# Kernel optimization log

Hardware: AMD Instinct MI355X
Metric: run time of the kernel (lower is better)

Reference implementation:

```python
import jax, jax.numpy as jnp
import numpy as np

B, S, D, H = 4, 2048, 512, 8
HD = D // H
SCALE = jnp.sqrt(jnp.float32(HD))


def setup_inputs() -> dict:
    key = jax.random.key(0)
    ks = jax.random.split(key, 13)
    s = 0.02
    return {
        "Q": jax.random.normal(ks[0], (B, S, D), jnp.float32),
        "K": jax.random.normal(ks[1], (B, S, D), jnp.float32),
        "V": jax.random.normal(ks[2], (B, S, D), jnp.float32),
        "mask": jax.random.randint(ks[3], (B, 1, S, S), 0, 2).astype(bool),
        "Wq": jax.random.normal(ks[4], (D, D), jnp.float32) * s,
        "bq": jnp.zeros((D,), jnp.float32),
        "Wk": jax.random.normal(ks[5], (D, D), jnp.float32) * s,
        "bk": jnp.zeros((D,), jnp.float32),
        "Wv": jax.random.normal(ks[6], (D, D), jnp.float32) * s,
        "bv": jnp.zeros((D,), jnp.float32),
        "Wo": jax.random.normal(ks[7], (D, D), jnp.float32) * s,
        "bo": jnp.zeros((D,), jnp.float32),
    }


def reference(Q, K, V, mask, Wq, bq, Wk, bk, Wv, bv, Wo, bo):
    b, s, d = Q.shape
    # torch Linear: x @ W^T + b
    q = (Q @ Wq.T + bq).reshape(b, s, H, HD).transpose(0, 2, 1, 3)  # [B,H,S,HD]
    k = (K @ Wk.T + bk).reshape(b, s, H, HD).transpose(0, 2, 1, 3)
    v = (V @ Wv.T + bv).reshape(b, s, H, HD).transpose(0, 2, 1, 3)
    scores = jnp.einsum('bhqd,bhkd->bhqk', q, k) / SCALE  # [B,H,S,S]
    scores = jnp.where(mask, jnp.float32(-1e10), scores)
    dist = jax.nn.softmax(scores, axis=-1)
    attn = jnp.einsum('bhqk,bhkd->bhqd', dist, v)
    x = attn.transpose(0, 2, 1, 3).reshape(b, s, d)
    x = x @ Wo.T + bo
    return x, dist
```

## Files before the change

kernel.cpp:

```cpp
#include <hip/hip_runtime.h>
#include <hip/hip_bf16.h>
#include <math.h>

#define B 4
#define S 2048
#define D 512
#define H 8
#define HD 64
#define M_TOT (B * S)
#define X_SIZE (B * S * D)
#define STRIDE_BH (S * HD)
#define STRIDE_B (H * S * HD)
#define SW64 (S / 64)

typedef __attribute__((ext_vector_type(8))) short bf16x8;
typedef __attribute__((ext_vector_type(4))) float f32x4;

__global__ __launch_bounds__(256) void cvt_all(
    const float* __restrict__ Q, const float* __restrict__ K,
    const float* __restrict__ V, const float* __restrict__ Wq,
    const float* __restrict__ Wk, const float* __restrict__ Wv,
    const float* __restrict__ Wo, __hip_bfloat16* __restrict__ outb) {
  const int NX = X_SIZE / 8;
  const int NW = (D * D) / 8;
  const int total = 3 * NX + 4 * NW;
  int c = blockIdx.x * 256 + threadIdx.x;
  const int stride = gridDim.x * 256;
  for (; c < total; c += stride) {
    const float* src;
    int off;
    if (c < NX)          { src = Q;  off = c; }
    else if (c < 2 * NX) { src = K;  off = c - NX; }
    else if (c < 3 * NX) { src = V;  off = c - 2 * NX; }
    else {
      int wc = c - 3 * NX;
      int wi = wc >> 15;
      src = (wi == 0) ? Wq : (wi == 1) ? Wk : (wi == 2) ? Wv : Wo;
      off = wc & (NW - 1);
    }
    const float4 x0 = *(const float4*)&src[(size_t)off * 8];
    const float4 x1 = *(const float4*)&src[(size_t)off * 8 + 4];
    bf16x8 pk;
    __hip_bfloat16* p = (__hip_bfloat16*)&pk;
    p[0] = __float2bfloat16(x0.x); p[1] = __float2bfloat16(x0.y);
    p[2] = __float2bfloat16(x0.z); p[3] = __float2bfloat16(x0.w);
    p[4] = __float2bfloat16(x1.x); p[5] = __float2bfloat16(x1.y);
    p[6] = __float2bfloat16(x1.z); p[7] = __float2bfloat16(x1.w);
    *(bf16x8*)&outb[(size_t)c * 8] = pk;
  }
}

__global__ __launch_bounds__(256) void mask_pack(
    const int* __restrict__ mask, unsigned long long* __restrict__ mbits) {
  const int lane = threadIdx.x & 63;
  const int wid = threadIdx.x >> 6;
  const size_t nwords = (size_t)B * S * SW64;
  size_t w = (size_t)blockIdx.x * 4 + wid;
  const size_t stride = (size_t)gridDim.x * 4;
  for (; w < nwords; w += stride) {
    int m = mask[w * 64 + lane];
    unsigned long long bits = __ballot(m != 0);
    if (lane == 0) mbits[w] = bits;
  }
}

template <int TRANS>
__global__ __launch_bounds__(256) void gemm_proj(
    const __hip_bfloat16* __restrict__ X, const __hip_bfloat16* __restrict__ W,
    const float* __restrict__ bias, __hip_bfloat16* __restrict__ out) {
  __shared__ __hip_bfloat16 As[64][72];
  __shared__ __hip_bfloat16 Bs[64][72];
  const int tid = threadIdx.x;
  const int lane = tid & 63;
  const int wave = tid >> 6;
  const int wr = wave >> 1, wc = wave & 1;
  const int l15 = lane & 15, quad = lane >> 4;
  const int h = blockIdx.x;
  const int n0 = h * 64;
  const int m0 = blockIdx.y * 64;

  f32x4 acc[2][2] = {};

  for (int k0 = 0; k0 < D; k0 += 64) {
#pragma unroll
    for (int i = 0; i < 2; ++i) {
      int idx = tid + i * 256;
      int r = idx >> 3, c8 = idx & 7;
      *(bf16x8*)&As[r][c8 * 8] = *(const bf16x8*)&X[(size_t)(m0 + r) * D + k0 + c8 * 8];
      *(bf16x8*)&Bs[r][c8 * 8] = *(const bf16x8*)&W[(size_t)(n0 + r) * D + k0 + c8 * 8];
    }
    __syncthreads();

    bf16x8 a[2][2], b[2][2];
#pragma unroll
    for (int mf = 0; mf < 2; ++mf) {
      a[mf][0] = *(const bf16x8*)&As[wr * 32 + mf * 16 + l15][quad * 8];
      a[mf][1] = *(const bf16x8*)&As[wr * 32 + mf * 16 + l15][32 + quad * 8];
    }
#pragma unroll
    for (int nf = 0; nf < 2; ++nf) {
      b[nf][0] = *(const bf16x8*)&Bs[wc * 32 + nf * 16 + l15][quad * 8];
      b[nf][1] = *(const bf16x8*)&Bs[wc * 32 + nf * 16 + l15][32 + quad * 8];
    }
#pragma unroll
    for (int mf = 0; mf < 2; ++mf)
#pragma unroll
      for (int nf = 0; nf < 2; ++nf) {
        if (TRANS) {
          acc[mf][nf] = __builtin_amdgcn_mfma_f32_16x16x32_bf16(b[nf][0], a[mf][0], acc[mf][nf], 0, 0, 0);
          acc[mf][nf] = __builtin_amdgcn_mfma_f32_16x16x32_bf16(b[nf][1], a[mf][1], acc[mf][nf], 0, 0, 0);
        } else {
          acc[mf][nf] = __builtin_amdgcn_mfma_f32_16x16x32_bf16(a[mf][0], b[nf][0], acc[mf][nf], 0, 0, 0);
          acc[mf][nf] = __builtin_amdgcn_mfma_f32_16x16x32_bf16(a[mf][1], b[nf][1], acc[mf][nf], 0, 0, 0);
        }
      }
    __syncthreads();
  }

  if (!TRANS) {
#pragma unroll
    for (int mf = 0; mf < 2; ++mf)
#pragma unroll
      for (int r = 0; r < 4; ++r) {
        int m = m0 + wr * 32 + mf * 16 + quad * 4 + r;
        int bb = m >> 11, s = m & 2047;
        __hip_bfloat16* obh = out + (size_t)bb * STRIDE_B + (size_t)h * STRIDE_BH;
#pragma unroll
        for (int nf = 0; nf < 2; ++nf) {
          int hd = wc * 32 + nf * 16 + l15;
          obh[(size_t)s * HD + hd] =
              __float2bfloat16(acc[mf][nf][r] + bias[n0 + hd]);
        }
      }
  } else {
#pragma unroll
    for (int mf = 0; mf < 2; ++mf)
#pragma unroll
      for (int r = 0; r < 4; ++r)
#pragma unroll
        for (int nf = 0; nf < 2; ++nf) {
          int hd = wc * 32 + nf * 16 + quad * 4 + r;
          int m = m0 + wr * 32 + mf * 16 + l15;
          int bb = m >> 11, s = m & 2047;
          __hip_bfloat16* obh = out + (size_t)bb * STRIDE_B + (size_t)h * STRIDE_BH;
          obh[(size_t)hd * S + s] =
              __float2bfloat16(acc[mf][nf][r] + bias[n0 + hd]);
        }
  }
}

__global__ __launch_bounds__(256) void attn_fused(
    const __hip_bfloat16* __restrict__ q, const __hip_bfloat16* __restrict__ k,
    const __hip_bfloat16* __restrict__ vT,
    const unsigned long long* __restrict__ mbits,
    float* __restrict__ dist, __hip_bfloat16* __restrict__ attn) {
  __shared__ __hip_bfloat16 ps[4][16][72];

  const int tid = threadIdx.x;
  const int wave = tid >> 6;
  const int lane = tid & 63;
  const int l15 = lane & 15;
  const int quad = lane >> 4;
  const int qt = blockIdx.x >> 5;
  const int bh = blockIdx.x & 31;
  const int b = bh >> 3;
  const int row0 = qt * 64 + wave * 16;

  const __hip_bfloat16* qb  = q  + (size_t)bh * STRIDE_BH;
  const __hip_bfloat16* kb  = k  + (size_t)bh * STRIDE_BH;
  const __hip_bfloat16* vtb = vT + (size_t)bh * STRIDE_BH;
  const unsigned long long* mb64 = mbits + (size_t)b * S * SW64;
  float* distb = dist + (size_t)bh * S * S;
  __hip_bfloat16* af = attn + (size_t)b * S * D + (size_t)(bh & 7) * HD;

  const bf16x8 qf0 = *(const bf16x8*)(qb + (size_t)(row0 + l15) * HD + quad * 8);
  const bf16x8 qf1 = *(const bf16x8*)(qb + (size_t)(row0 + l15) * HD + 32 + quad * 8);

  float lpart[4] = {0.f, 0.f, 0.f, 0.f};

  for (int kt = 0; kt < 32; ++kt) {
    const int col0 = kt * 64;
    unsigned long long mw[4];
#pragma unroll
    for (int r = 0; r < 4; ++r)
      mw[r] = mb64[(size_t)(row0 + quad * 4 + r) * SW64 + kt];
#pragma unroll
    for (int ct = 0; ct < 4; ++ct) {
      const int col = col0 + ct * 16 + l15;
      const bf16x8 kf0 = *(const bf16x8*)(kb + (size_t)col * HD + quad * 8);
      const bf16x8 kf1 = *(const bf16x8*)(kb + (size_t)col * HD + 32 + quad * 8);
      f32x4 s = {0.f, 0.f, 0.f, 0.f};
      s = __builtin_amdgcn_mfma_f32_16x16x32_bf16(qf0, kf0, s, 0, 0, 0);
      s = __builtin_amdgcn_mfma_f32_16x16x32_bf16(qf1, kf1, s, 0, 0, 0);
#pragma unroll
      for (int r = 0; r < 4; ++r) {
        int msk = (int)((mw[r] >> (ct * 16 + l15)) & 1ull);
        float e = msk ? 0.f : __expf(s[r] * 0.125f);
        lpart[r] += e;
      }
    }
  }
#pragma unroll
  for (int r = 0; r < 4; ++r) {
    float v = lpart[r];
    v += __shfl_xor(v, 1, 64);
    v += __shfl_xor(v, 2, 64);
    v += __shfl_xor(v, 4, 64);
    v += __shfl_xor(v, 8, 64);
    lpart[r] = 1.0f / v;
  }

  f32x4 oacc[4] = {{0.f, 0.f, 0.f, 0.f}, {0.f, 0.f, 0.f, 0.f},
                   {0.f, 0.f, 0.f, 0.f}, {0.f, 0.f, 0.f, 0.f}};
  for (int kt = 0; kt < 32; ++kt) {
    const int col0 = kt * 64;
    unsigned long long mw[4];
#pragma unroll
    for (int r = 0; r < 4; ++r)
      mw[r] = mb64[(size_t)(row0 + quad * 4 + r) * SW64 + kt];
#pragma unroll
    for (int ct = 0; ct < 4; ++ct) {
      const int col = col0 + ct * 16 + l15;
      const bf16x8 kf0 = *(const bf16x8*)(kb + (size_t)col * HD + quad * 8);
      const bf16x8 kf1 = *(const bf16x8*)(kb + (size_t)col * HD + 32 + quad * 8);
      f32x4 s = {0.f, 0.f, 0.f, 0.f};
      s = __builtin_amdgcn_mfma_f32_16x16x32_bf16(qf0, kf0, s, 0, 0, 0);
      s = __builtin_amdgcn_mfma_f32_16x16x32_bf16(qf1, kf1, s, 0, 0, 0);
#pragma unroll
      for (int r = 0; r < 4; ++r) {
        int row = row0 + quad * 4 + r;
        int msk = (int)((mw[r] >> (ct * 16 + l15)) & 1ull);
        float e = msk ? 0.f : __expf(s[r] * 0.125f);
        float p = e * lpart[r];
        __builtin_nontemporal_store(p, &distb[(size_t)row * S + col]);
        ps[wave][quad * 4 + r][ct * 16 + l15] = __float2bfloat16(p);
      }
    }
    const bf16x8 pa0 = *(const bf16x8*)&ps[wave][l15][quad * 8];
    const bf16x8 pa1 = *(const bf16x8*)&ps[wave][l15][32 + quad * 8];
#pragma unroll
    for (int ct = 0; ct < 4; ++ct) {
      const __hip_bfloat16* vrow = vtb + (size_t)(ct * 16 + l15) * S + col0;
      const bf16x8 vf0 = *(const bf16x8*)(vrow + quad * 8);
      const bf16x8 vf1 = *(const bf16x8*)(vrow + 32 + quad * 8);
      oacc[ct] = __builtin_amdgcn_mfma_f32_16x16x32_bf16(pa0, vf0, oacc[ct], 0, 0, 0);
      oacc[ct] = __builtin_amdgcn_mfma_f32_16x16x32_bf16(pa1, vf1, oacc[ct], 0, 0, 0);
    }
  }

#pragma unroll
  for (int ct = 0; ct < 4; ++ct)
#pragma unroll
    for (int r = 0; r < 4; ++r) {
      int row = row0 + quad * 4 + r;
      af[(size_t)row * D + ct * 16 + l15] = __float2bfloat16(oacc[ct][r]);
    }
}

__global__ __launch_bounds__(256) void gemm_out(
    const __hip_bfloat16* __restrict__ Abf, const __hip_bfloat16* __restrict__ W,
    const float* __restrict__ bias, float* __restrict__ outp) {
  __shared__ __hip_bfloat16 As[64][72];
  __shared__ __hip_bfloat16 Bs[64][72];
  const int tid = threadIdx.x;
  const int lane = tid & 63;
  const int wave = tid >> 6;
  const int wr = wave >> 1, wc = wave & 1;
  const int l15 = lane & 15, quad = lane >> 4;
  const int n0 = blockIdx.x * 64;
  const int m0 = blockIdx.y * 64;

  f32x4 acc[2][2] = {};

  for (int k0 = 0; k0 < D; k0 += 64) {
#pragma unroll
    for (int i = 0; i < 2; ++i) {
      int idx = tid + i * 256;
      int r = idx >> 3, c8 = idx & 7;
      *(bf16x8*)&As[r][c8 * 8] = *(const bf16x8*)&Abf[(size_t)(m0 + r) * D + k0 + c8 * 8];
      *(bf16x8*)&Bs[r][c8 * 8] = *(const bf16x8*)&W[(size_t)(n0 + r) * D + k0 + c8 * 8];
    }
    __syncthreads();

    bf16x8 a[2][2], b[2][2];
#pragma unroll
    for (int mf = 0; mf < 2; ++mf) {
      a[mf][0] = *(const bf16x8*)&As[wr * 32 + mf * 16 + l15][quad * 8];
      a[mf][1] = *(const bf16x8*)&As[wr * 32 + mf * 16 + l15][32 + quad * 8];
    }
#pragma unroll
    for (int nf = 0; nf < 2; ++nf) {
      b[nf][0] = *(const bf16x8*)&Bs[wc * 32 + nf * 16 + l15][quad * 8];
      b[nf][1] = *(const bf16x8*)&Bs[wc * 32 + nf * 16 + l15][32 + quad * 8];
    }
#pragma unroll
    for (int mf = 0; mf < 2; ++mf)
#pragma unroll
      for (int nf = 0; nf < 2; ++nf) {
        acc[mf][nf] = __builtin_amdgcn_mfma_f32_16x16x32_bf16(a[mf][0], b[nf][0], acc[mf][nf], 0, 0, 0);
        acc[mf][nf] = __builtin_amdgcn_mfma_f32_16x16x32_bf16(a[mf][1], b[nf][1], acc[mf][nf], 0, 0, 0);
      }
    __syncthreads();
  }

#pragma unroll
  for (int mf = 0; mf < 2; ++mf)
#pragma unroll
    for (int r = 0; r < 4; ++r) {
      int m = m0 + wr * 32 + mf * 16 + quad * 4 + r;
#pragma unroll
      for (int nf = 0; nf < 2; ++nf) {
        int n = n0 + wc * 32 + nf * 16 + l15;
        outp[(size_t)m * D + n] = acc[mf][nf][r] + bias[n];
      }
    }
}

extern "C" void kernel_launch(void* const* d_in, const int* in_sizes, int n_in,
                              void* d_out, int out_size, void* d_ws, size_t ws_size,
                              hipStream_t stream) {
  const float* Q    = (const float*)d_in[0];
  const float* K    = (const float*)d_in[1];
  const float* V    = (const float*)d_in[2];
  const int*   mask = (const int*)d_in[3];
  const float* Wq   = (const float*)d_in[4];
  const float* bq   = (const float*)d_in[5];
  const float* Wk   = (const float*)d_in[6];
  const float* bk   = (const float*)d_in[7];
  const float* Wv   = (const float*)d_in[8];
  const float* bv   = (const float*)d_in[9];
  const float* Wo   = (const float*)d_in[10];
  const float* bo   = (const float*)d_in[11];

  float* x_out = (float*)d_out;
  float* dist  = x_out + (size_t)X_SIZE;

  __hip_bfloat16* cvtb = (__hip_bfloat16*)d_ws;
  __hip_bfloat16* Qb   = cvtb;
  __hip_bfloat16* Kb   = Qb + (size_t)X_SIZE;
  __hip_bfloat16* Vb   = Kb + (size_t)X_SIZE;
  __hip_bfloat16* Wqb  = Vb + (size_t)X_SIZE;
  __hip_bfloat16* Wkb  = Wqb + (size_t)D * D;
  __hip_bfloat16* Wvb  = Wkb + (size_t)D * D;
  __hip_bfloat16* Wob  = Wvb + (size_t)D * D;
  __hip_bfloat16* qb   = Wob + (size_t)D * D;
  __hip_bfloat16* kbf  = qb + (size_t)X_SIZE;
  __hip_bfloat16* vtb  = kbf + (size_t)X_SIZE;
  unsigned long long* mbits = (unsigned long long*)(vtb + (size_t)X_SIZE);
  __hip_bfloat16* abf  = Qb;

  dim3 blk(256);
  dim3 g(D / 64, M_TOT / 64);

  cvt_all<<<dim3(2048), blk, 0, stream>>>(Q, K, V, Wq, Wk, Wv, Wo, cvtb);
  mask_pack<<<dim3(1024), blk, 0, stream>>>(mask, mbits);
  gemm_proj<0><<<g, blk, 0, stream>>>(Qb, Wqb, bq, qb);
  gemm_proj<0><<<g, blk, 0, stream>>>(Kb, Wkb, bk, kbf);
  gemm_proj<1><<<g, blk, 0, stream>>>(Vb, Wvb, bv, vtb);
  attn_fused<<<dim3(B * H * S / 64), blk, 0, stream>>>(qb, kbf, vtb, mbits, dist, abf);
  gemm_out<<<g, blk, 0, stream>>>(abf, Wob, bo, x_out);
}
```

Measured before the change: 1.018 ms.

## Stage K/V tiles in LDS with async loads, merge QKV GEMMs, prefetch GEMM tiles

The attention kernel now double-buffers K and V^T tiles in XOR-swizzled shared memory using global_load_lds, so the four waves of a block share one copy instead of each reading K/V from global memory. The P tile layout is also swizzled to avoid bank conflicts. The three projection GEMMs are merged into one launch over a z-dimension, and both GEMM kernels prefetch the next K-slice into registers while computing the current one. These changes aim to cut redundant global traffic and launch overhead, at the cost of extra barriers per tile and a runtime branch on trans inside the merged kernel.

Result: faster. 889.9 us (-12.5%).

```diff
diff --git a/kernel.cpp b/kernel.cpp
--- a/kernel.cpp
+++ b/kernel.cpp
@@ -15,6 +15,12 @@
 
 typedef __attribute__((ext_vector_type(8))) short bf16x8;
 typedef __attribute__((ext_vector_type(4))) float f32x4;
+
+__device__ __forceinline__ void gld_lds16(const void* g, void* l) {
+  __builtin_amdgcn_global_load_lds(
+      (const __attribute__((address_space(1))) unsigned int*)g,
+      (__attribute__((address_space(3))) unsigned int*)l, 16, 0, 0);
+}
 
 __global__ __launch_bounds__(256) void cvt_all(
     const float* __restrict__ Q, const float* __restrict__ K,
@@ -64,12 +70,19 @@
   }
 }
 
-template <int TRANS>
-__global__ __launch_bounds__(256) void gemm_proj(
-    const __hip_bfloat16* __restrict__ X, const __hip_bfloat16* __restrict__ W,
-    const float* __restrict__ bias, __hip_bfloat16* __restrict__ out) {
+__global__ __launch_bounds__(256) void gemm_qkv(
+    const __hip_bfloat16* __restrict__ Xall, const __hip_bfloat16* __restrict__ Wall,
+    const float* __restrict__ bq, const float* __restrict__ bk,
+    const float* __restrict__ bv, __hip_bfloat16* __restrict__ outall) {
   __shared__ __hip_bfloat16 As[64][72];
   __shared__ __hip_bfloat16 Bs[64][72];
+  const int z = blockIdx.z;
+  const __hip_bfloat16* X = Xall + (size_t)z * X_SIZE;
+  const __hip_bfloat16* W = Wall + (size_t)z * (D * D);
+  const float* bias = (z == 0) ? bq : (z == 1) ? bk : bv;
+  __hip_bfloat16* out = outall + (size_t)z * X_SIZE;
+  const bool trans = (z == 2);
+
   const int tid = threadIdx.x;
   const int lane = tid & 63;
   const int wave = tid >> 6;
@@ -78,19 +91,30 @@
   const int h = blockIdx.x;
   const int n0 = h * 64;
   const int m0 = blockIdx.y * 64;
-
+  const int r_ = tid >> 3, c8 = tid & 7;
+
+  bf16x8 xr[2], wv[2];
+#pragma unroll
+  for (int i = 0; i < 2; ++i) {
+    xr[i] = *(const bf16x8*)&X[(size_t)(m0 + r_ + i * 32) * D + c8 * 8];
+    wv[i] = *(const bf16x8*)&W[(size_t)(n0 + r_ + i * 32) * D + c8 * 8];
+  }
   f32x4 acc[2][2] = {};
 
   for (int k0 = 0; k0 < D; k0 += 64) {
 #pragma unroll
     for (int i = 0; i < 2; ++i) {
-      int idx = tid + i * 256;
-      int r = idx >> 3, c8 = idx & 7;
-      *(bf16x8*)&As[r][c8 * 8] = *(const bf16x8*)&X[(size_t)(m0 + r) * D + k0 + c8 * 8];
-      *(bf16x8*)&Bs[r][c8 * 8] = *(const bf16x8*)&W[(size_t)(n0 + r) * D + k0 + c8 * 8];
-    }
-    __syncthreads();
-
+      *(bf16x8*)&As[r_ + i * 32][c8 * 8] = xr[i];
+      *(bf16x8*)&Bs[r_ + i * 32][c8 * 8] = wv[i];
+    }
+    __syncthreads();
+    if (k0 + 64 < D) {
+#pragma unroll
+      for (int i = 0; i < 2; ++i) {
+        xr[i] = *(const bf16x8*)&X[(size_t)(m0 + r_ + i * 32) * D + (k0 + 64) + c8 * 8];
+        wv[i] = *(const bf16x8*)&W[(size_t)(n0 + r_ + i * 32) * D + (k0 + 64) + c8 * 8];
+      }
+    }
     bf16x8 a[2][2], b[2][2];
 #pragma unroll
     for (int mf = 0; mf < 2; ++mf) {
@@ -102,22 +126,27 @@
       b[nf][0] = *(const bf16x8*)&Bs[wc * 32 + nf * 16 + l15][quad * 8];
       b[nf][1] = *(const bf16x8*)&Bs[wc * 32 + nf * 16 + l15][32 + quad * 8];
     }
-#pragma unroll
-    for (int mf = 0; mf < 2; ++mf)
-#pragma unroll
-      for (int nf = 0; nf < 2; ++nf) {
-        if (TRANS) {
+    if (trans) {
+#pragma unroll
+      for (int mf = 0; mf < 2; ++mf)
+#pragma unroll
+        for (int nf = 0; nf < 2; ++nf) {
           acc[mf][nf] = __builtin_amdgcn_mfma_f32_16x16x32_bf16(b[nf][0], a[mf][0], acc[mf][nf], 0, 0, 0);
           acc[mf][nf] = __builtin_amdgcn_mfma_f32_16x16x32_bf16(b[nf][1], a[mf][1], acc[mf][nf], 0, 0, 0);
-        } else {
+        }
+    } else {
+#pragma unroll
+      for (int mf = 0; mf < 2; ++mf)
+#pragma unroll
+        for (int nf = 0; nf < 2; ++nf) {
           acc[mf][nf] = __builtin_amdgcn_mfma_f32_16x16x32_bf16(a[mf][0], b[nf][0], acc[mf][nf], 0, 0, 0);
           acc[mf][nf] = __builtin_amdgcn_mfma_f32_16x16x32_bf16(a[mf][1], b[nf][1], acc[mf][nf], 0, 0, 0);
         }
-      }
-    __syncthreads();
-  }
-
-  if (!TRANS) {
+    }
+    __syncthreads();
+  }
+
+  if (!trans) {
 #pragma unroll
     for (int mf = 0; mf < 2; ++mf)
 #pragma unroll
@@ -128,8 +157,7 @@
 #pragma unroll
         for (int nf = 0; nf < 2; ++nf) {
           int hd = wc * 32 + nf * 16 + l15;
-          obh[(size_t)s * HD + hd] =
-              __float2bfloat16(acc[mf][nf][r] + bias[n0 + hd]);
+          obh[(size_t)s * HD + hd] = __float2bfloat16(acc[mf][nf][r] + bias[n0 + hd]);
         }
       }
   } else {
@@ -143,8 +171,7 @@
           int m = m0 + wr * 32 + mf * 16 + l15;
           int bb = m >> 11, s = m & 2047;
           __hip_bfloat16* obh = out + (size_t)bb * STRIDE_B + (size_t)h * STRIDE_BH;
-          obh[(size_t)hd * S + s] =
-              __float2bfloat16(acc[mf][nf][r] + bias[n0 + hd]);
+          obh[(size_t)hd * S + s] = __float2bfloat16(acc[mf][nf][r] + bias[n0 + hd]);
         }
   }
 }
@@ -154,13 +181,18 @@
     const __hip_bfloat16* __restrict__ vT,
     const unsigned long long* __restrict__ mbits,
     float* __restrict__ dist, __hip_bfloat16* __restrict__ attn) {
-  __shared__ __hip_bfloat16 ps[4][16][72];
+  __shared__ __hip_bfloat16 Kt[2][64][64];
+  __shared__ __hip_bfloat16 Vt[2][64][64];
+  __shared__ __hip_bfloat16 ps[4][16][64];
 
   const int tid = threadIdx.x;
   const int wave = tid >> 6;
   const int lane = tid & 63;
   const int l15 = lane & 15;
   const int quad = lane >> 4;
+  const int sw = l15 & 7;
+  const int c0q = (quad ^ sw) << 3;
+  const int c1q = ((4 | quad) ^ sw) << 3;
   const int qt = blockIdx.x >> 5;
   const int bh = blockIdx.x & 31;
   const int b = bh >> 3;
@@ -173,22 +205,43 @@
   float* distb = dist + (size_t)bh * S * S;
   __hip_bfloat16* af = attn + (size_t)b * S * D + (size_t)(bh & 7) * HD;
 
+  const int sr = lane >> 3;
+  const int schunk = ((lane & 7) ^ sr) * 16;
+
   const bf16x8 qf0 = *(const bf16x8*)(qb + (size_t)(row0 + l15) * HD + quad * 8);
   const bf16x8 qf1 = *(const bf16x8*)(qb + (size_t)(row0 + l15) * HD + 32 + quad * 8);
 
+  auto stageK = [&](int buf, int kt) {
+    const char* g0 = (const char*)(kb + (size_t)(kt * 64 + wave * 16) * HD);
+#pragma unroll
+    for (int hh = 0; hh < 2; ++hh)
+      gld_lds16(g0 + (size_t)(hh * 8 + sr) * 128 + schunk,
+                &Kt[buf][wave * 16 + hh * 8][0]);
+  };
+  auto stageV = [&](int buf, int kt) {
+    const char* g0 = (const char*)(vtb + (size_t)(wave * 16) * S + kt * 64);
+#pragma unroll
+    for (int hh = 0; hh < 2; ++hh)
+      gld_lds16(g0 + (size_t)(hh * 8 + sr) * (S * 2) + schunk,
+                &Vt[buf][wave * 16 + hh * 8][0]);
+  };
+
   float lpart[4] = {0.f, 0.f, 0.f, 0.f};
 
+  stageK(0, 0);
+  __syncthreads();
   for (int kt = 0; kt < 32; ++kt) {
-    const int col0 = kt * 64;
+    const int buf = kt & 1;
+    if (kt < 31) stageK(buf ^ 1, kt + 1);
     unsigned long long mw[4];
 #pragma unroll
     for (int r = 0; r < 4; ++r)
       mw[r] = mb64[(size_t)(row0 + quad * 4 + r) * SW64 + kt];
 #pragma unroll
     for (int ct = 0; ct < 4; ++ct) {
-      const int col = col0 + ct * 16 + l15;
-      const bf16x8 kf0 = *(const bf16x8*)(kb + (size_t)col * HD + quad * 8);
-      const bf16x8 kf1 = *(const bf16x8*)(kb + (size_t)col * HD + 32 + quad * 8);
+      const __hip_bfloat16* Krow = &Kt[buf][ct * 16 + l15][0];
+      const bf16x8 kf0 = *(const bf16x8*)(Krow + c0q);
+      const bf16x8 kf1 = *(const bf16x8*)(Krow + c1q);
       f32x4 s = {0.f, 0.f, 0.f, 0.f};
       s = __builtin_amdgcn_mfma_f32_16x16x32_bf16(qf0, kf0, s, 0, 0, 0);
       s = __builtin_amdgcn_mfma_f32_16x16x32_bf16(qf1, kf1, s, 0, 0, 0);
@@ -199,6 +252,7 @@
         lpart[r] += e;
       }
     }
+    __syncthreads();
   }
 #pragma unroll
   for (int r = 0; r < 4; ++r) {
@@ -212,7 +266,12 @@
 
   f32x4 oacc[4] = {{0.f, 0.f, 0.f, 0.f}, {0.f, 0.f, 0.f, 0.f},
                    {0.f, 0.f, 0.f, 0.f}, {0.f, 0.f, 0.f, 0.f}};
+  stageK(0, 0);
+  stageV(0, 0);
+  __syncthreads();
   for (int kt = 0; kt < 32; ++kt) {
+    const int buf = kt & 1;
+    if (kt < 31) { stageK(buf ^ 1, kt + 1); stageV(buf ^ 1, kt + 1); }
     const int col0 = kt * 64;
     unsigned long long mw[4];
 #pragma unroll
@@ -220,9 +279,9 @@
       mw[r] = mb64[(size_t)(row0 + quad * 4 + r) * SW64 + kt];
 #pragma unroll
     for (int ct = 0; ct < 4; ++ct) {
-      const int col = col0 + ct * 16 + l15;
-      const bf16x8 kf0 = *(const bf16x8*)(kb + (size_t)col * HD + quad * 8);
-      const bf16x8 kf1 = *(const bf16x8*)(kb + (size_t)col * HD + 32 + quad * 8);
+      const __hip_bfloat16* Krow = &Kt[buf][ct * 16 + l15][0];
+      const bf16x8 kf0 = *(const bf16x8*)(Krow + c0q);
+      const bf16x8 kf1 = *(const bf16x8*)(Krow + c1q);
       f32x4 s = {0.f, 0.f, 0.f, 0.f};
       s = __builtin_amdgcn_mfma_f32_16x16x32_bf16(qf0, kf0, s, 0, 0, 0);
       s = __builtin_amdgcn_mfma_f32_16x16x32_bf16(qf1, kf1, s, 0, 0, 0);
@@ -232,20 +291,23 @@
         int msk = (int)((mw[r] >> (ct * 16 + l15)) & 1ull);
         float e = msk ? 0.f : __expf(s[r] * 0.125f);
         float p = e * lpart[r];
-        __builtin_nontemporal_store(p, &distb[(size_t)row * S + col]);
-        ps[wave][quad * 4 + r][ct * 16 + l15] = __float2bfloat16(p);
-      }
-    }
-    const bf16x8 pa0 = *(const bf16x8*)&ps[wave][l15][quad * 8];
-    const bf16x8 pa1 = *(const bf16x8*)&ps[wave][l15][32 + quad * 8];
+        __builtin_nontemporal_store(p, &distb[(size_t)row * S + col0 + ct * 16 + l15]);
+        int prow = quad * 4 + r;
+        int chunk = (ct * 2 + (l15 >> 3)) ^ (prow & 7);
+        ps[wave][prow][chunk * 8 + (l15 & 7)] = __float2bfloat16(p);
+      }
+    }
+    const bf16x8 pa0 = *(const bf16x8*)&ps[wave][l15][c0q];
+    const bf16x8 pa1 = *(const bf16x8*)&ps[wave][l15][c1q];
 #pragma unroll
     for (int ct = 0; ct < 4; ++ct) {
-      const __hip_bfloat16* vrow = vtb + (size_t)(ct * 16 + l15) * S + col0;
-      const bf16x8 vf0 = *(const bf16x8*)(vrow + quad * 8);
-      const bf16x8 vf1 = *(const bf16x8*)(vrow + 32 + quad * 8);
+      const __hip_bfloat16* Vrow = &Vt[buf][ct * 16 + l15][0];
+      const bf16x8 vf0 = *(const bf16x8*)(Vrow + c0q);
+      const bf16x8 vf1 = *(const bf16x8*)(Vrow + c1q);
       oacc[ct] = __builtin_amdgcn_mfma_f32_16x16x32_bf16(pa0, vf0, oacc[ct], 0, 0, 0);
       oacc[ct] = __builtin_amdgcn_mfma_f32_16x16x32_bf16(pa1, vf1, oacc[ct], 0, 0, 0);
     }
+    __syncthreads();
   }
 
 #pragma unroll
@@ -269,19 +331,30 @@
   const int l15 = lane & 15, quad = lane >> 4;
   const int n0 = blockIdx.x * 64;
   const int m0 = blockIdx.y * 64;
-
+  const int r_ = tid >> 3, c8 = tid & 7;
+
+  bf16x8 xr[2], wv[2];
+#pragma unroll
+  for (int i = 0; i < 2; ++i) {
+    xr[i] = *(const bf16x8*)&Abf[(size_t)(m0 + r_ + i * 32) * D + c8 * 8];
+    wv[i] = *(const bf16x8*)&W[(size_t)(n0 + r_ + i * 32) * D + c8 * 8];
+  }
   f32x4 acc[2][2] = {};
 
   for (int k0 = 0; k0 < D; k0 += 64) {
 #pragma unroll
     for (int i = 0; i < 2; ++i) {
-      int idx = tid + i * 256;
-      int r = idx >> 3, c8 = idx & 7;
-      *(bf16x8*)&As[r][c8 * 8] = *(const bf16x8*)&Abf[(size_t)(m0 + r) * D + k0 + c8 * 8];
-      *(bf16x8*)&Bs[r][c8 * 8] = *(const bf16x8*)&W[(size_t)(n0 + r) * D + k0 + c8 * 8];
-    }
-    __syncthreads();
-
+      *(bf16x8*)&As[r_ + i * 32][c8 * 8] = xr[i];
+      *(bf16x8*)&Bs[r_ + i * 32][c8 * 8] = wv[i];
+    }
+    __syncthreads();
+    if (k0 + 64 < D) {
+#pragma unroll
+      for (int i = 0; i < 2; ++i) {
+        xr[i] = *(const bf16x8*)&Abf[(size_t)(m0 + r_ + i * 32) * D + (k0 + 64) + c8 * 8];
+        wv[i] = *(const bf16x8*)&W[(size_t)(n0 + r_ + i * 32) * D + (k0 + 64) + c8 * 8];
+      }
+    }
     bf16x8 a[2][2], b[2][2];
 #pragma unroll
     for (int mf = 0; mf < 2; ++mf) {
@@ -337,12 +410,8 @@
 
   __hip_bfloat16* cvtb = (__hip_bfloat16*)d_ws;
   __hip_bfloat16* Qb   = cvtb;
-  __hip_bfloat16* Kb   = Qb + (size_t)X_SIZE;
-  __hip_bfloat16* Vb   = Kb + (size_t)X_SIZE;
-  __hip_bfloat16* Wqb  = Vb + (size_t)X_SIZE;
-  __hip_bfloat16* Wkb  = Wqb + (size_t)D * D;
-  __hip_bfloat16* Wvb  = Wkb + (size_t)D * D;
-  __hip_bfloat16* Wob  = Wvb + (size_t)D * D;
+  __hip_bfloat16* Wqb  = Qb + (size_t)3 * X_SIZE;
+  __hip_bfloat16* Wob  = Wqb + (size_t)3 * D * D;
   __hip_bfloat16* qb   = Wob + (size_t)D * D;
   __hip_bfloat16* kbf  = qb + (size_t)X_SIZE;
   __hip_bfloat16* vtb  = kbf + (size_t)X_SIZE;
@@ -350,13 +419,10 @@
   __hip_bfloat16* abf  = Qb;
 
   dim3 blk(256);
-  dim3 g(D / 64, M_TOT / 64);
 
   cvt_all<<<dim3(2048), blk, 0, stream>>>(Q, K, V, Wq, Wk, Wv, Wo, cvtb);
   mask_pack<<<dim3(1024), blk, 0, stream>>>(mask, mbits);
-  gemm_proj<0><<<g, blk, 0, stream>>>(Qb, Wqb, bq, qb);
-  gemm_proj<0><<<g, blk, 0, stream>>>(Kb, Wkb, bk, kbf);
-  gemm_proj<1><<<g, blk, 0, stream>>>(Vb, Wvb, bv, vtb);
+  gemm_qkv<<<dim3(D / 64, M_TOT / 64, 3), blk, 0, stream>>>(Qb, Wqb, bq, bk, bv, qb);
   attn_fused<<<dim3(B * H * S / 64), blk, 0, stream>>>(qb, kbf, vtb, mbits, dist, abf);
-  gemm_out<<<g, blk, 0, stream>>>(abf, Wob, bo, x_out);
-}
+  gemm_out<<<dim3(D / 64, M_TOT / 64), blk, 0, stream>>>(abf, Wob, bo, x_out);
+}
```
